# Optimization experiments

Measured on AMD Instinct MI355X. Metric: run time of the kernel, lower is better.

## Reference

```python
import jax, jax.numpy as jnp
import numpy as np

VOCAB = 50257
HID = 1024
SEQ = 2048


def setup_inputs() -> dict:
    key = jax.random.key(0)
    ks = jax.random.split(key, 12)
    s = 0.02
    return {
        "input_token": jax.random.randint(ks[0], (1,), 0, VOCAB),
        "hidden": jax.random.normal(ks[1], (1, 1, HID), jnp.float32),
        "encoder_outputs": jax.random.normal(ks[2], (SEQ, 1, HID), jnp.float32),
        "emb": jax.random.normal(ks[3], (VOCAB, HID), jnp.float32) * s,
        "attn_W": jax.random.normal(ks[4], (2 * HID, HID), jnp.float32) * s,
        "attn_v": jax.random.normal(ks[5], (HID,), jnp.float32) * s,
        "W_ih": jax.random.normal(ks[6], (3 * HID, 2 * HID), jnp.float32) * s,
        "b_ih": jax.random.normal(ks[7], (3 * HID,), jnp.float32) * s,
        "W_hh": jax.random.normal(ks[8], (3 * HID, HID), jnp.float32) * s,
        "b_hh": jax.random.normal(ks[9], (3 * HID,), jnp.float32) * s,
        "out_W": jax.random.normal(ks[10], (VOCAB, HID), jnp.float32) * s,
        "out_b": jax.random.normal(ks[11], (VOCAB,), jnp.float32) * s,
    }


def reference(input_token, hidden, encoder_outputs, emb, attn_W, attn_v,
              W_ih, b_ih, W_hh, b_hh, out_W, out_b):
    H = hidden.shape[-1]
    embedded = emb[input_token[0]]                 # [H]  (embedding lookup, view(1,1,-1))
    h_last = hidden[-1, 0]                         # [H]  hidden[-1], batch=1
    enc = encoder_outputs[:, 0]                    # [S,H]
    S = enc.shape[0]
    # additive attention: softmax(v^T tanh(Wa [h; enc_s]))
    feat = jnp.concatenate([jnp.broadcast_to(h_last, (S, H)), enc], axis=1)  # [S,2H]
    scores = jnp.tanh(feat @ attn_W) @ attn_v      # [S]
    w = jax.nn.softmax(scores)                     # [S]
    context = w @ enc                              # [H]  (bmm of [1,1,S] x [1,S,H])
    x = jnp.concatenate([embedded, context])       # [2H] gru_input
    # PyTorch GRU cell math (gate order r,z,n)
    gi = W_ih @ x + b_ih                           # [3H]
    gh = W_hh @ h_last + b_hh                      # [3H]
    ir, iz, inn = jnp.split(gi, 3)
    hr, hz, hn = jnp.split(gh, 3)
    r = jax.nn.sigmoid(ir + hr)
    z = jax.nn.sigmoid(iz + hz)
    n = jnp.tanh(inn + r * hn)
    h_new = (1.0 - z) * n + z * h_last             # [H]
    logits = out_W @ h_new + out_b                 # [V]
    out = jax.nn.log_softmax(logits)[None, :]      # [1,V]
    return out, h_new[None, None, :]               # ([1,V], [1,1,H])
```

## Files before the change

kernel.cpp:

```cpp
#include <hip/hip_runtime.h>
#include <math.h>

#define HID 1024
#define SEQ 2048
#define VOCAB 50257

__global__ __launch_bounds__(256) void k_init(const int* tok, const float* emb,
                                              float* x, float* hW, float* scores) {
    int tid = threadIdx.x;
    size_t ebase = (size_t)tok[0] * HID;
#pragma unroll
    for (int q = 0; q < 4; ++q) {
        int j = q * 256 + tid;
        x[j] = emb[ebase + j];
        x[1024 + j] = 0.f;
        hW[j] = 0.f;
    }
#pragma unroll
    for (int q = 0; q < 8; ++q) scores[q * 256 + tid] = 0.f;
}

__global__ __launch_bounds__(256) void k_hw(const float* __restrict__ hidden,
                                            const float* __restrict__ attn_W,
                                            float* hW) {
    int j0 = threadIdx.x * 4;
    int k0 = blockIdx.x * 16;
    float4 acc = {0.f, 0.f, 0.f, 0.f};
#pragma unroll 4
    for (int k = k0; k < k0 + 16; ++k) {
        float h = hidden[k];
        float4 w = *(const float4*)(attn_W + (size_t)k * HID + j0);
        acc.x += h * w.x; acc.y += h * w.y; acc.z += h * w.z; acc.w += h * w.w;
    }
    atomicAdd(&hW[j0 + 0], acc.x);
    atomicAdd(&hW[j0 + 1], acc.y);
    atomicAdd(&hW[j0 + 2], acc.z);
    atomicAdd(&hW[j0 + 3], acc.w);
}

__global__ __launch_bounds__(256) void k_gh(const float* __restrict__ hidden,
                                            const float* __restrict__ W_hh,
                                            const float* __restrict__ b_hh,
                                            float* gh) {
    int wid = threadIdx.x >> 6, lane = threadIdx.x & 63;
    int row = blockIdx.x * 4 + wid;
    const float* wr = W_hh + (size_t)row * HID;
    float acc = 0.f;
#pragma unroll
    for (int it = 0; it < 4; ++it) {
        float4 wv = *(const float4*)(wr + it * 256 + lane * 4);
        float4 hv = *(const float4*)(hidden + it * 256 + lane * 4);
        acc += wv.x * hv.x + wv.y * hv.y + wv.z * hv.z + wv.w * hv.w;
    }
    for (int off = 32; off; off >>= 1) acc += __shfl_down(acc, off);
    if (lane == 0) gh[row] = acc + b_hh[row];
}

#define TS 8
#define JSPLIT 4
__global__ __launch_bounds__(256) void k_scores(const float* __restrict__ enc,
                                                const float* __restrict__ attn_W,
                                                const float* __restrict__ hW,
                                                const float* __restrict__ attn_v,
                                                float* __restrict__ scores) {
    __shared__ float red[4][TS];
    int st = blockIdx.x / JSPLIT;
    int jb = blockIdx.x % JSPLIT;
    int s0 = st * TS;
    int j  = jb * 256 + threadIdx.x;
    const float* __restrict__ Wb   = attn_W + (size_t)HID * HID;
    const float* __restrict__ erow = enc + (size_t)s0 * HID;

    float acc[TS];
#pragma unroll
    for (int ss = 0; ss < TS; ++ss) acc[ss] = 0.f;

#pragma unroll 4
    for (int k = 0; k < HID; ++k) {
        float w = Wb[(size_t)k * HID + j];
#pragma unroll
        for (int ss = 0; ss < TS; ++ss)
            acc[ss] += erow[(size_t)ss * HID + k] * w;
    }

    float hw = hW[j], v = attn_v[j];
    int wid = threadIdx.x >> 6, lane = threadIdx.x & 63;
#pragma unroll
    for (int ss = 0; ss < TS; ++ss) {
        float p = tanhf(hw + acc[ss]) * v;
        for (int off = 32; off; off >>= 1) p += __shfl_down(p, off);
        if (lane == 0) red[wid][ss] = p;
    }
    __syncthreads();
    if (threadIdx.x < TS)
        atomicAdd(&scores[s0 + threadIdx.x],
                  red[0][threadIdx.x] + red[1][threadIdx.x]
                + red[2][threadIdx.x] + red[3][threadIdx.x]);
}

__global__ __launch_bounds__(1024) void k_softmax(const float* scores, float* wts) {
    __shared__ float red[16];
    int tid = threadIdx.x, wid = tid >> 6, lane = tid & 63;
    float a = scores[tid], b = scores[tid + 1024];
    float m = fmaxf(a, b);
    for (int off = 32; off; off >>= 1) m = fmaxf(m, __shfl_xor(m, off));
    if (lane == 0) red[wid] = m;
    __syncthreads();
    float M = red[0];
#pragma unroll
    for (int q = 1; q < 16; ++q) M = fmaxf(M, red[q]);
    __syncthreads();
    float ea = expf(a - M), eb = expf(b - M);
    float s = ea + eb;
    for (int off = 32; off; off >>= 1) s += __shfl_xor(s, off);
    if (lane == 0) red[wid] = s;
    __syncthreads();
    float S = 0.f;
#pragma unroll
    for (int q = 0; q < 16; ++q) S += red[q];
    float inv = 1.f / S;
    wts[tid] = ea * inv;
    wts[tid + 1024] = eb * inv;
}

__global__ __launch_bounds__(256) void k_context(const float* __restrict__ enc,
                                                 const float* __restrict__ wts,
                                                 float* x) {
    int b = blockIdx.x;
    int j0 = threadIdx.x * 4;
    float4 acc = {0.f, 0.f, 0.f, 0.f};
    for (int s = b * 32; s < b * 32 + 32; ++s) {
        float wv = wts[s];
        float4 e = *(const float4*)(enc + (size_t)s * HID + j0);
        acc.x += wv * e.x; acc.y += wv * e.y; acc.z += wv * e.z; acc.w += wv * e.w;
    }
    atomicAdd(&x[1024 + j0 + 0], acc.x);
    atomicAdd(&x[1024 + j0 + 1], acc.y);
    atomicAdd(&x[1024 + j0 + 2], acc.z);
    atomicAdd(&x[1024 + j0 + 3], acc.w);
}

__global__ __launch_bounds__(256) void k_gi(const float* __restrict__ W_ih,
                                            const float* __restrict__ b_ih,
                                            const float* __restrict__ x, float* gi) {
    __shared__ float red[4];
    int b = blockIdx.x;
    int wid = threadIdx.x >> 6, lane = threadIdx.x & 63;
    int row = b * 2 + (wid >> 1);
    int half = wid & 1;
    const float* wr = W_ih + (size_t)row * 2048 + half * 1024;
    const float* xr = x + half * 1024;
    float acc = 0.f;
#pragma unroll
    for (int it = 0; it < 4; ++it) {
        float4 wv = *(const float4*)(wr + it * 256 + lane * 4);
        float4 xv = *(const float4*)(xr + it * 256 + lane * 4);
        acc += wv.x * xv.x + wv.y * xv.y + wv.z * xv.z + wv.w * xv.w;
    }
    for (int off = 32; off; off >>= 1) acc += __shfl_down(acc, off);
    if (lane == 0) red[wid] = acc;
    __syncthreads();
    if (threadIdx.x < 2) {
        int r = b * 2 + threadIdx.x;
        gi[r] = red[threadIdx.x * 2] + red[threadIdx.x * 2 + 1] + b_ih[r];
    }
}

__global__ __launch_bounds__(256) void k_gru(const float* gi, const float* gh,
                                             const float* hidden, float* hn,
                                             float* out) {
    int i = blockIdx.x * 256 + threadIdx.x;
    float r = 1.f / (1.f + expf(-(gi[i] + gh[i])));
    float z = 1.f / (1.f + expf(-(gi[1024 + i] + gh[1024 + i])));
    float n = tanhf(gi[2048 + i] + r * gh[2048 + i]);
    float h = (1.f - z) * n + z * hidden[i];
    hn[i] = h;
    out[VOCAB + i] = h;
}

__global__ __launch_bounds__(256) void k_logits(const float* __restrict__ out_W,
                                                const float* __restrict__ out_b,
                                                const float* __restrict__ hn,
                                                float* logits, float* pm, float* psum) {
    __shared__ float lg[4];
    int b = blockIdx.x;
    int wid = threadIdx.x >> 6, lane = threadIdx.x & 63;
    int row = b * 4 + wid;
    float logit = -INFINITY;
    if (row < VOCAB) {
        const float* wr = out_W + (size_t)row * HID;
        float acc = 0.f;
#pragma unroll
        for (int it = 0; it < 4; ++it) {
            float4 wv = *(const float4*)(wr + it * 256 + lane * 4);
            float4 hv = *(const float4*)(hn + it * 256 + lane * 4);
            acc += wv.x * hv.x + wv.y * hv.y + wv.z * hv.z + wv.w * hv.w;
        }
        for (int off = 32; off; off >>= 1) acc += __shfl_down(acc, off);
        if (lane == 0) {
            logit = acc + out_b[row];
            logits[row] = logit;
        }
    }
    if (lane == 0) lg[wid] = logit;
    __syncthreads();
    if (threadIdx.x == 0) {
        float m = fmaxf(fmaxf(lg[0], lg[1]), fmaxf(lg[2], lg[3]));
        float s = 0.f;
#pragma unroll
        for (int q = 0; q < 4; ++q)
            if (lg[q] != -INFINITY) s += expf(lg[q] - m);
        pm[b] = m;
        psum[b] = s;
    }
}

__global__ __launch_bounds__(256) void k_combine(const float* pm, const float* psum,
                                                 int n, float* Lval) {
    __shared__ float rm[4], rs[4];
    int tid = threadIdx.x, wid = tid >> 6, lane = tid & 63;
    float m = -INFINITY, s = 0.f;
    for (int i = tid; i < n; i += 256) {
        float bm = pm[i], bs = psum[i];
        float M = fmaxf(m, bm);
        s = s * expf(m - M) + bs * expf(bm - M);
        m = M;
    }
    for (int off = 32; off; off >>= 1) {
        float om = __shfl_xor(m, off), os = __shfl_xor(s, off);
        float M = fmaxf(m, om);
        s = s * expf(m - M) + os * expf(om - M);
        m = M;
    }
    if (lane == 0) { rm[wid] = m; rs[wid] = s; }
    __syncthreads();
    if (tid == 0) {
        float M = fmaxf(fmaxf(rm[0], rm[1]), fmaxf(rm[2], rm[3]));
        float S = rs[0] * expf(rm[0] - M) + rs[1] * expf(rm[1] - M)
                + rs[2] * expf(rm[2] - M) + rs[3] * expf(rm[3] - M);
        Lval[0] = M + logf(S);
    }
}

__global__ __launch_bounds__(256) void k_final(const float* logits, const float* Lval,
                                               float* out) {
    int i = blockIdx.x * 256 + threadIdx.x;
    if (i < VOCAB) out[i] = logits[i] - Lval[0];
}

extern "C" void kernel_launch(void* const* d_in, const int* in_sizes, int n_in,
                              void* d_out, int out_size, void* d_ws, size_t ws_size,
                              hipStream_t stream) {
    (void)in_sizes; (void)n_in; (void)out_size; (void)ws_size;
    const int*   tok    = (const int*)d_in[0];
    const float* hidden = (const float*)d_in[1];
    const float* enc    = (const float*)d_in[2];
    const float* emb    = (const float*)d_in[3];
    const float* attn_W = (const float*)d_in[4];
    const float* attn_v = (const float*)d_in[5];
    const float* W_ih   = (const float*)d_in[6];
    const float* b_ih   = (const float*)d_in[7];
    const float* W_hh   = (const float*)d_in[8];
    const float* b_hh   = (const float*)d_in[9];
    const float* out_W  = (const float*)d_in[10];
    const float* out_b  = (const float*)d_in[11];
    float* out = (float*)d_out;
    float* ws  = (float*)d_ws;

    float* hW     = ws + 0;
    float* gh     = ws + 1024;
    float* gi     = ws + 4096;
    float* x      = ws + 7168;
    float* scores = ws + 9216;
    float* wts    = ws + 11264;
    float* hn     = ws + 13312;
    float* logits = ws + 14336;
    float* pm     = ws + 64600;
    float* psum   = ws + 77168;
    float* Lval   = ws + 89736;

    const int NLOGB = (VOCAB + 3) / 4;

    k_init   <<<1, 256, 0, stream>>>(tok, emb, x, hW, scores);
    k_hw     <<<64, 256, 0, stream>>>(hidden, attn_W, hW);
    k_gh     <<<768, 256, 0, stream>>>(hidden, W_hh, b_hh, gh);
    k_scores <<<(SEQ / TS) * JSPLIT, 256, 0, stream>>>(enc, attn_W, hW, attn_v, scores);
    k_softmax<<<1, 1024, 0, stream>>>(scores, wts);
    k_context<<<64, 256, 0, stream>>>(enc, wts, x);
    k_gi     <<<1536, 256, 0, stream>>>(W_ih, b_ih, x, gi);
    k_gru    <<<4, 256, 0, stream>>>(gi, gh, hidden, hn, out);
    k_logits <<<NLOGB, 256, 0, stream>>>(out_W, out_b, hn, logits, pm, psum);
    k_combine<<<1, 256, 0, stream>>>(pm, psum, NLOGB, Lval);
    k_final  <<<(VOCAB + 255) / 256, 256, 0, stream>>>(logits, Lval, out);
}
```

Before: 598.8 us.

## Compute attention scores with bf16 MFMA GEMM over transposed bf16 weights

Replaces the scalar FP32 attention-score kernel with two kernels. The first transposes the encoder half of attn_W and converts it to bf16. The second is a tiled bf16 MFMA GEMM of encoder outputs against those weights, with a fused tanh, v-dot and atomic reduction into the scores. This removes the per-thread FMA loop over 2048x1024x1024 that dominated runtime, at the cost of reduced bf16 input precision and an extra transpose pass over the weight matrix on every call.

Result: faster. 489.5 us (-18.2%).

```diff
diff --git a/kernel.cpp b/kernel.cpp
--- a/kernel.cpp
+++ b/kernel.cpp
@@ -4,6 +4,15 @@
 #define HID 1024
 #define SEQ 2048
 #define VOCAB 50257
+
+typedef unsigned int  uint;
+typedef unsigned short ushort_t;
+
+__device__ __forceinline__ ushort_t f2bf(float f) {
+    uint u = __float_as_uint(f);
+    uint r = (u + 0x7FFFu + ((u >> 16) & 1u)) >> 16;
+    return (ushort_t)r;
+}
 
 __global__ __launch_bounds__(256) void k_init(const int* tok, const float* emb,
                                               float* x, float* hW, float* scores) {
@@ -56,46 +65,115 @@
     if (lane == 0) gh[row] = acc + b_hh[row];
 }
 
-#define TS 8
-#define JSPLIT 4
-__global__ __launch_bounds__(256) void k_scores(const float* __restrict__ enc,
-                                                const float* __restrict__ attn_W,
-                                                const float* __restrict__ hW,
-                                                const float* __restrict__ attn_v,
-                                                float* __restrict__ scores) {
-    __shared__ float red[4][TS];
-    int st = blockIdx.x / JSPLIT;
-    int jb = blockIdx.x % JSPLIT;
-    int s0 = st * TS;
-    int j  = jb * 256 + threadIdx.x;
-    const float* __restrict__ Wb   = attn_W + (size_t)HID * HID;
-    const float* __restrict__ erow = enc + (size_t)s0 * HID;
-
-    float acc[TS];
-#pragma unroll
-    for (int ss = 0; ss < TS; ++ss) acc[ss] = 0.f;
-
-#pragma unroll 4
-    for (int k = 0; k < HID; ++k) {
-        float w = Wb[(size_t)k * HID + j];
-#pragma unroll
-        for (int ss = 0; ss < TS; ++ss)
-            acc[ss] += erow[(size_t)ss * HID + k] * w;
-    }
-
-    float hw = hW[j], v = attn_v[j];
-    int wid = threadIdx.x >> 6, lane = threadIdx.x & 63;
-#pragma unroll
-    for (int ss = 0; ss < TS; ++ss) {
-        float p = tanhf(hw + acc[ss]) * v;
-        for (int off = 32; off; off >>= 1) p += __shfl_down(p, off);
-        if (lane == 0) red[wid][ss] = p;
-    }
-    __syncthreads();
-    if (threadIdx.x < TS)
-        atomicAdd(&scores[s0 + threadIdx.x],
-                  red[0][threadIdx.x] + red[1][threadIdx.x]
-                + red[2][threadIdx.x] + red[3][threadIdx.x]);
+__global__ __launch_bounds__(256) void k_transW(const float* __restrict__ attn_W,
+                                                ushort_t* __restrict__ WT) {
+    __shared__ ushort_t T[64][68];
+    const float* Wb = attn_W + (size_t)HID * HID;
+    int bx = blockIdx.x & 15;
+    int by = blockIdx.x >> 4;
+    int j0 = bx * 64, k0 = by * 64;
+    int t = threadIdx.x;
+    int kk = t >> 4;
+    int jj = (t & 15) * 4;
+#pragma unroll
+    for (int p = 0; p < 4; ++p) {
+        int k = kk + p * 16;
+        float4 wv = *(const float4*)(Wb + (size_t)(k0 + k) * HID + j0 + jj);
+        ushort4 u;
+        u.x = f2bf(wv.x); u.y = f2bf(wv.y); u.z = f2bf(wv.z); u.w = f2bf(wv.w);
+        *(ushort4*)&T[k][jj] = u;
+    }
+    __syncthreads();
+    int j = t >> 2, g = t & 3;
+#pragma unroll
+    for (int half = 0; half < 2; ++half) {
+        int kc = g * 8 + half * 32;
+        ushort_t tmp[8];
+#pragma unroll
+        for (int e = 0; e < 8; ++e) tmp[e] = T[kc + e][j];
+        uint4 o;
+        o.x = (uint)tmp[0] | ((uint)tmp[1] << 16);
+        o.y = (uint)tmp[2] | ((uint)tmp[3] << 16);
+        o.z = (uint)tmp[4] | ((uint)tmp[5] << 16);
+        o.w = (uint)tmp[6] | ((uint)tmp[7] << 16);
+        *(uint4*)(WT + (size_t)(j0 + j) * HID + k0 + kc) = o;
+    }
+}
+
+typedef __attribute__((ext_vector_type(8))) short bf16x8;
+typedef __attribute__((ext_vector_type(4))) float f32x4;
+
+__global__ __launch_bounds__(256) void k_gemm(const float* __restrict__ enc,
+                                              const ushort_t* __restrict__ WT,
+                                              const float* __restrict__ hW,
+                                              const float* __restrict__ attn_v,
+                                              float* __restrict__ scores) {
+    __shared__ ushort_t As[64][40];
+    __shared__ ushort_t Bs[64][40];
+    int bj = blockIdx.x & 15;
+    int bs = blockIdx.x >> 4;
+    int s0 = bs * 64, j0 = bj * 64;
+    int t = threadIdx.x, l = t & 63, w = t >> 6;
+    int sr = t >> 2;
+    int sp = (t & 3) * 8;
+    int cl = l & 15;
+    int kq = l >> 4;
+    int ac = kq * 8;
+
+    f32x4 acc0 = {0,0,0,0}, acc1 = {0,0,0,0}, acc2 = {0,0,0,0}, acc3 = {0,0,0,0};
+
+    for (int ks = 0; ks < HID / 32; ++ks) {
+        int k0 = ks * 32;
+        const float* ap = enc + (size_t)(s0 + sr) * HID + k0 + sp;
+        float4 a0 = *(const float4*)(ap);
+        float4 a1 = *(const float4*)(ap + 4);
+        uint4 ua;
+        ua.x = (uint)f2bf(a0.x) | ((uint)f2bf(a0.y) << 16);
+        ua.y = (uint)f2bf(a0.z) | ((uint)f2bf(a0.w) << 16);
+        ua.z = (uint)f2bf(a1.x) | ((uint)f2bf(a1.y) << 16);
+        ua.w = (uint)f2bf(a1.z) | ((uint)f2bf(a1.w) << 16);
+        *(uint4*)&As[sr][sp] = ua;
+        uint4 ub = *(const uint4*)(WT + (size_t)(j0 + sr) * HID + k0 + sp);
+        *(uint4*)&Bs[sr][sp] = ub;
+        __syncthreads();
+
+        bf16x8 af = *(const bf16x8*)&As[16 * w + cl][ac];
+        bf16x8 b0 = *(const bf16x8*)&Bs[ 0 + cl][ac];
+        bf16x8 b1 = *(const bf16x8*)&Bs[16 + cl][ac];
+        bf16x8 b2 = *(const bf16x8*)&Bs[32 + cl][ac];
+        bf16x8 b3 = *(const bf16x8*)&Bs[48 + cl][ac];
+        acc0 = __builtin_amdgcn_mfma_f32_16x16x32_bf16(af, b0, acc0, 0, 0, 0);
+        acc1 = __builtin_amdgcn_mfma_f32_16x16x32_bf16(af, b1, acc1, 0, 0, 0);
+        acc2 = __builtin_amdgcn_mfma_f32_16x16x32_bf16(af, b2, acc2, 0, 0, 0);
+        acc3 = __builtin_amdgcn_mfma_f32_16x16x32_bf16(af, b3, acc3, 0, 0, 0);
+        __syncthreads();
+    }
+
+    float part0 = 0.f, part1 = 0.f, part2 = 0.f, part3 = 0.f;
+#pragma unroll
+    for (int jt = 0; jt < 4; ++jt) {
+        int j = j0 + jt * 16 + cl;
+        float hwj = hW[j], vj = attn_v[j];
+        f32x4 a = (jt == 0) ? acc0 : (jt == 1) ? acc1 : (jt == 2) ? acc2 : acc3;
+        part0 += tanhf(hwj + a[0]) * vj;
+        part1 += tanhf(hwj + a[1]) * vj;
+        part2 += tanhf(hwj + a[2]) * vj;
+        part3 += tanhf(hwj + a[3]) * vj;
+    }
+#pragma unroll
+    for (int m = 1; m <= 8; m <<= 1) {
+        part0 += __shfl_xor(part0, m);
+        part1 += __shfl_xor(part1, m);
+        part2 += __shfl_xor(part2, m);
+        part3 += __shfl_xor(part3, m);
+    }
+    if (cl == 0) {
+        int srow = s0 + 16 * w + 4 * kq;
+        atomicAdd(&scores[srow + 0], part0);
+        atomicAdd(&scores[srow + 1], part1);
+        atomicAdd(&scores[srow + 2], part2);
+        atomicAdd(&scores[srow + 3], part3);
+    }
 }
 
 __global__ __launch_bounds__(1024) void k_softmax(const float* scores, float* wts) {
@@ -278,13 +356,15 @@
     float* pm     = ws + 64600;
     float* psum   = ws + 77168;
     float* Lval   = ws + 89736;
+    ushort_t* WT  = (ushort_t*)(ws + 90112);
 
     const int NLOGB = (VOCAB + 3) / 4;
 
     k_init   <<<1, 256, 0, stream>>>(tok, emb, x, hW, scores);
     k_hw     <<<64, 256, 0, stream>>>(hidden, attn_W, hW);
     k_gh     <<<768, 256, 0, stream>>>(hidden, W_hh, b_hh, gh);
-    k_scores <<<(SEQ / TS) * JSPLIT, 256, 0, stream>>>(enc, attn_W, hW, attn_v, scores);
+    k_transW <<<256, 256, 0, stream>>>(attn_W, WT);
+    k_gemm   <<<512, 256, 0, stream>>>(enc, WT, hW, attn_v, scores);
     k_softmax<<<1, 1024, 0, stream>>>(scores, wts);
     k_context<<<64, 256, 0, stream>>>(enc, wts, x);
     k_gi     <<<1536, 256, 0, stream>>>(W_ih, b_ih, x, gi);
```
